# Optimization experiments

Measured on AMD Instinct MI355X. Metric: run time of the kernel, lower is better.

## Reference

```python
import jax, jax.numpy as jnp
import numpy as np

B, H, W, C = 16, 96, 96, 128
FOCAL_LEVEL = 3
FOCAL_WINDOW = 3
FOCAL_FACTOR = 2
LN_EPS = 1e-3  # keras LayerNormalization default epsilon


def dwconv_same(x, k):
    # x: [B,H,W,C], k: [kh,kw,1,C] depthwise kernel (feature_group_count=C)
    return jax.lax.conv_general_dilated(
        x, k, window_strides=(1, 1), padding='SAME',
        dimension_numbers=('NHWC', 'HWIO', 'NHWC'),
        feature_group_count=x.shape[-1])


def setup_inputs() -> dict:
    key = jax.random.key(0)
    ks = jax.random.split(key, 12)
    s = 0.02
    out_f = 2 * C + (FOCAL_LEVEL + 1)
    inp = {
        'x': jax.random.normal(ks[0], (B, H, W, C), dtype=jnp.float32),
        'Wf': jax.random.normal(ks[1], (C, out_f), dtype=jnp.float32) * s,
        'bf': jnp.zeros((out_f,), dtype=jnp.float32),
        'Wh': jax.random.normal(ks[2], (C, C), dtype=jnp.float32) * s,
        'bh': jnp.zeros((C,), dtype=jnp.float32),
        'gamma': jnp.ones((C,), dtype=jnp.float32),
        'beta': jnp.zeros((C,), dtype=jnp.float32),
        'Wp': jax.random.normal(ks[3], (C, C), dtype=jnp.float32) * s,
        'bp': jnp.zeros((C,), dtype=jnp.float32),
    }
    for l in range(FOCAL_LEVEL):
        kk = FOCAL_FACTOR * l + FOCAL_WINDOW  # 3, 5, 7
        inp[f'k{l}'] = jax.random.normal(ks[4 + l], (kk, kk, 1, C), dtype=jnp.float32) * s
    return inp


def reference(x, Wf, bf, k0, k1, k2, Wh, bh, gamma, beta, Wp, bp):
    gelu = lambda t: jax.nn.gelu(t, approximate=False)  # keras gelu is exact
    y = jnp.einsum('bhwc,cd->bhwd', x, Wf) + bf  # f(): [B,H,W,2C+L+1]
    q = y[..., :C]
    ctx = y[..., C:2 * C]
    gates = y[..., 2 * C:]  # [B,H,W,L+1]

    ctx_all = jnp.zeros_like(ctx)
    for l, k in enumerate((k0, k1, k2)):
        ctx = gelu(dwconv_same(ctx, k))
        ctx_all = ctx_all + ctx * gates[..., l:l + 1]

    ctx_global = gelu(jnp.mean(ctx, axis=(1, 2), keepdims=True))  # [B,1,1,C]
    ctx_all = ctx_all + ctx_global * gates[..., FOCAL_LEVEL:]

    modulator = jnp.einsum('bhwc,cd->bhwd', ctx_all, Wh) + bh  # 1x1 conv h()
    x_out = q * modulator

    # post-LN over channel dim
    mu = jnp.mean(x_out, axis=-1, keepdims=True)
    var = jnp.mean(jnp.square(x_out - mu), axis=-1, keepdims=True)
    x_out = (x_out - mu) * jax.lax.rsqrt(var + LN_EPS) * gamma + beta

    x_out = jnp.einsum('bhwc,cd->bhwd', x_out, Wp) + bp  # proj (dropout p=0)
    return x_out
```

## Files before the change

### kernel.cpp

```cpp
#include <hip/hip_runtime.h>
#include <math.h>

#define B_ 16
#define H_ 96
#define W_ 96
#define C_ 128
#define HW_ (H_*W_)
#define NTOK (B_*HW_)
#define NOUT 260

#define TH 16
#define TW 32
#define B0H 28
#define B0W 44
#define B1H 26
#define B1W 42
#define B2H 22
#define B2W 38

typedef unsigned short ushort_t;
typedef unsigned int uint_t;
typedef float f32x4 __attribute__((ext_vector_type(4)));
typedef float f32x2 __attribute__((ext_vector_type(2)));
typedef short bfrag __attribute__((ext_vector_type(8)));
typedef unsigned short us8 __attribute__((ext_vector_type(8)));

__device__ __forceinline__ float gelu_f(float t) {
    return 0.5f * t * (1.0f + erff(t * 0.7071067811865475f));
}
__device__ __forceinline__ float b2f(ushort_t u) {
    union { unsigned int i; float f; } t; t.i = (unsigned int)u << 16; return t.f;
}
__device__ __forceinline__ ushort_t f2b(float f) {
    union { float f; unsigned int i; } t; t.f = f;
    unsigned int lsb = (t.i >> 16) & 1u;
    t.i += 0x7fffu + lsb;
    return (ushort_t)(t.i >> 16);
}
__device__ __forceinline__ void unp2(uint_t u, float& a, float& b) {
    union { unsigned int i; float f; } x, y;
    x.i = u << 16; y.i = u & 0xffff0000u;
    a = x.f; b = y.f;
}
__device__ __forceinline__ void unp8(const uint4 v, float* f) {
    unp2(v.x, f[0], f[1]); unp2(v.y, f[2], f[3]);
    unp2(v.z, f[4], f[5]); unp2(v.w, f[6], f[7]);
}
__device__ __forceinline__ uint_t pk2(float a, float b) {
    return (uint_t)f2b(a) | ((uint_t)f2b(b) << 16);
}
__device__ __forceinline__ uint4 pk8(const float* f) {
    uint4 v;
    v.x = pk2(f[0], f[1]); v.y = pk2(f[2], f[3]);
    v.z = pk2(f[4], f[5]); v.w = pk2(f[6], f[7]);
    return v;
}
__device__ __forceinline__ f32x2 unp2p(uint_t u) {
    union { uint_t i; float f; } a, b;
    a.i = u << 16; b.i = u & 0xffff0000u;
    f32x2 r; r.x = a.f; r.y = b.f; return r;
}
__device__ __forceinline__ void unp8p(const uint4 v, f32x2* d) {
    d[0] = unp2p(v.x); d[1] = unp2p(v.y); d[2] = unp2p(v.z); d[3] = unp2p(v.w);
}

__device__ __forceinline__ void split8_to(const float* f,
                                          ushort_t* __restrict__ hdst,
                                          ushort_t* __restrict__ ldst) {
    us8 vh, vl;
    #pragma unroll
    for (int j = 0; j < 8; ++j) {
        const ushort_t h = f2b(f[j]);
        vh[j] = h;
        vl[j] = f2b(f[j] - b2f(h));
    }
    *(us8*)hdst = vh;
    *(us8*)ldst = vl;
}

__global__ __launch_bounds__(128) void pack_weights(
    const float* __restrict__ Wf, const float* __restrict__ Wh,
    const float* __restrict__ Wp, ushort_t* __restrict__ pk)
{
    const int n = blockIdx.x, mat = blockIdx.y, k = threadIdx.x;
    float v;
    if (mat == 0)      v = Wf[(size_t)k * NOUT + n];
    else if (mat == 1) v = Wf[(size_t)k * NOUT + C_ + n];
    else if (mat == 2) v = Wh[(size_t)k * C_ + n];
    else               v = Wp[(size_t)k * C_ + n];
    const ushort_t h = f2b(v);
    const ushort_t l = f2b(v - b2f(h));
    ushort_t* base = pk + (size_t)mat * (2 * C_ * C_);
    base[n * C_ + k] = h;
    base[C_ * C_ + n * C_ + k] = l;
}

template <bool A_LO>
__device__ __forceinline__ void mfma_gemm64(
    const ushort_t (*Ah)[136], const ushort_t (*Al)[136],
    const ushort_t* __restrict__ Bh, const ushort_t* __restrict__ Bl,
    int lane, int n0, f32x4 acc[4][2])
{
    const int ar = lane & 15;
    const int ak = (lane >> 4) << 3;
    #pragma unroll
    for (int kk = 0; kk < 4; ++kk) {
        const int kb = (kk << 5) + ak;
        const bfrag bh0 = *(const bfrag*)(Bh + (((n0      + ar) << 7) + kb));
        const bfrag bh1 = *(const bfrag*)(Bh + (((n0 + 16 + ar) << 7) + kb));
        const bfrag bl0 = *(const bfrag*)(Bl + (((n0      + ar) << 7) + kb));
        const bfrag bl1 = *(const bfrag*)(Bl + (((n0 + 16 + ar) << 7) + kb));
        #pragma unroll
        for (int m = 0; m < 4; ++m) {
            const bfrag ah = *(const bfrag*)&Ah[(m << 4) + ar][kb];
            if constexpr (A_LO) {
                const bfrag al = *(const bfrag*)&Al[(m << 4) + ar][kb];
                acc[m][0] = __builtin_amdgcn_mfma_f32_16x16x32_bf16(al, bh0, acc[m][0], 0, 0, 0);
                acc[m][1] = __builtin_amdgcn_mfma_f32_16x16x32_bf16(al, bh1, acc[m][1], 0, 0, 0);
            }
            acc[m][0] = __builtin_amdgcn_mfma_f32_16x16x32_bf16(ah, bl0, acc[m][0], 0, 0, 0);
            acc[m][1] = __builtin_amdgcn_mfma_f32_16x16x32_bf16(ah, bl1, acc[m][1], 0, 0, 0);
            acc[m][0] = __builtin_amdgcn_mfma_f32_16x16x32_bf16(ah, bh0, acc[m][0], 0, 0, 0);
            acc[m][1] = __builtin_amdgcn_mfma_f32_16x16x32_bf16(ah, bh1, acc[m][1], 0, 0, 0);
        }
    }
}

__device__ __forceinline__ void stage_split_f32(
    const float* __restrict__ src, int tid,
    ushort_t (*Ah)[136], ushort_t (*Al)[136])
{
    #pragma unroll
    for (int p = 0; p < 4; ++p) {
        const int i  = tid + (p << 8);
        const int t  = i >> 4;
        const int c8 = (i & 15) << 3;
        const float4 v0 = *(const float4*)(src + (size_t)t * C_ + c8);
        const float4 v1 = *(const float4*)(src + (size_t)t * C_ + c8 + 4);
        const float f[8] = {v0.x, v0.y, v0.z, v0.w, v1.x, v1.y, v1.z, v1.w};
        split8_to(f, &Ah[t][c8], &Al[t][c8]);
    }
}

__global__ __launch_bounds__(256) void gemm_ctx_gates_mfma(
    const float* __restrict__ x, const float* __restrict__ Wf,
    const float* __restrict__ bf, const ushort_t* __restrict__ pk,
    ushort_t* __restrict__ ctx, float* __restrict__ gates,
    float* __restrict__ csum)
{
    __shared__ ushort_t Abuf[2][64][136];
    const int tid  = threadIdx.x;
    const int tok0 = blockIdx.x * 64;
    const int lane = tid & 63;
    const int n0   = (tid >> 6) << 5;

    if (blockIdx.x < 8) csum[blockIdx.x * 256 + tid] = 0.0f;

    stage_split_f32(x + (size_t)tok0 * C_, tid, Abuf[0], Abuf[1]);
    __syncthreads();

    f32x4 acc[4][2] = {};
    {
        const ushort_t* Bh = pk + (size_t)1 * (2 * C_ * C_);
        const ushort_t* Bl = Bh + C_ * C_;
        mfma_gemm64<true>(Abuf[0], Abuf[1], Bh, Bl, lane, n0, acc);
    }

    {
        const int g = tid >> 6;
        float s = 0.f;
        #pragma unroll
        for (int k8 = 0; k8 < C_; k8 += 8) {
            const us8 vh = *(const us8*)&Abuf[0][lane][k8];
            const us8 vl = *(const us8*)&Abuf[1][lane][k8];
            #pragma unroll
            for (int j = 0; j < 8; ++j) {
                const float xv = b2f((ushort_t)vh[j]) + b2f((ushort_t)vl[j]);
                s += xv * Wf[(size_t)(k8 + j) * NOUT + 2*C_ + g];
            }
        }
        gates[(size_t)(tok0 + lane) * 4 + g] = s + bf[2*C_ + g];
    }
    __syncthreads();

    {
        const int ar = lane & 15;
        const int rg = (lane >> 4) << 2;
        #pragma unroll
        for (int n = 0; n < 2; ++n) {
            const int col = n0 + (n << 4) + ar;
            const float bias = bf[C_ + col];
            #pragma unroll
            for (int m = 0; m < 4; ++m)
                #pragma unroll
                for (int r = 0; r < 4; ++r)
                    Abuf[0][(m << 4) + rg + r][col] = f2b(acc[m][n][r] + bias);
        }
    }
    __syncthreads();

    #pragma unroll
    for (int p = 0; p < 4; ++p) {
        const int i  = tid + (p << 8);
        const int cg = i >> 6;
        const int t  = i & 63;
        *(uint4*)(ctx + (((size_t)cg * NTOK + tok0 + t) << 3))
            = *(const uint4*)&Abuf[0][t][cg << 3];
    }
}

__global__ __launch_bounds__(256, 4) void focal_conv_fused(
    const ushort_t* __restrict__ ctx_in,
    const float* __restrict__ k0w, const float* __restrict__ k1w,
    const float* __restrict__ k2w,
    const float* __restrict__ gates,
    ushort_t* __restrict__ ctx_all,
    float* __restrict__ csum)
{
    __shared__ uint4 bufA[B0H*B0W];
    __shared__ uint4 buf1[B1H*B1W];
    __shared__ float wts[(9+25+49)*8];

    const int tid  = threadIdx.x;
    const int cg   = blockIdx.x;
    const int tile = blockIdx.y;
    const int bb   = blockIdx.z;
    const int wt   = tile % 3, ht = tile / 3;
    const int c0   = cg << 3;
    const int h0   = ht * TH, w0 = wt * TW;

    if (tid < 166) {
        const int f = tid << 2;
        const float* src; int r;
        if (f < 72)       { r = f;       src = k0w; }
        else if (f < 272) { r = f - 72;  src = k1w; }
        else              { r = f - 272; src = k2w; }
        const int tap = r >> 3, off = r & 7;
        *(float4*)&wts[f] = *(const float4*)(src + tap * C_ + c0 + off);
    }

    const ushort_t* cin = ctx_in + (((size_t)cg * NTOK + (size_t)bb * HW_) << 3);
    for (int i = tid; i < B0H*B0W; i += 256) {
        const int r = i / B0W, q = i - r * B0W;
        const int hh = h0 - 6 + r, ww = w0 - 6 + q;
        uint4 v = make_uint4(0u, 0u, 0u, 0u);
        if ((unsigned)hh < (unsigned)H_ && (unsigned)ww < (unsigned)W_)
            v = *(const uint4*)(cin + ((size_t)(hh * W_ + ww) << 3));
        bufA[i] = v;
    }
    __syncthreads();

    {
        int iv[5], ecp[5], boff[5];
        #pragma unroll
        for (int p = 0; p < 5; ++p) {
            const int e = tid + (p << 8);
            iv[p] = (e < B1H*B1W);
            const int ec = iv[p] ? e : 0;
            ecp[p] = ec;
            boff[p] = (ec / B1W) * B0W + (ec % B1W);
        }
        f32x2 acc[5][4] = {};
        #pragma unroll 1
        for (int a = 0; a < 3; ++a) {
            #pragma unroll
            for (int b = 0; b < 3; ++b) {
                f32x2 wv[4];
                #pragma unroll
                for (int c = 0; c < 4; ++c)
                    wv[c] = *(const f32x2*)&wts[(a*3+b)*8 + 2*c];
                const int off = a * B0W + b;
                #pragma unroll
                for (int p = 0; p < 5; ++p) {
                    f32x2 d[4]; unp8p(bufA[boff[p] + off], d);
                    #pragma unroll
                    for (int c = 0; c < 4; ++c)
                        acc[p][c] = __builtin_elementwise_fma(d[c], wv[c], acc[p][c]);
                }
            }
        }
        __syncthreads();
        #pragma unroll
        for (int p = 0; p < 5; ++p) if (iv[p]) {
            float g[8];
            #pragma unroll
            for (int c = 0; c < 4; ++c) {
                g[2*c]   = gelu_f(acc[p][c].x);
                g[2*c+1] = gelu_f(acc[p][c].y);
            }
            buf1[ecp[p]] = pk8(g);
        }
    }
    __syncthreads();

    {
        int iv[4], ecp[4], boff[4];
        #pragma unroll
        for (int p = 0; p < 4; ++p) {
            const int e = tid + (p << 8);
            iv[p] = (e < B2H*B2W);
            const int ec = iv[p] ? e : 0;
            ecp[p] = ec;
            boff[p] = (ec / B2W) * B1W + (ec % B2W);
        }
        f32x2 acc[4][4] = {};
        #pragma unroll 1
        for (int a = 0; a < 5; ++a) {
            #pragma unroll
            for (int b = 0; b < 5; ++b) {
                f32x2 wv[4];
                #pragma unroll
                for (int c = 0; c < 4; ++c)
                    wv[c] = *(const f32x2*)&wts[72 + (a*5+b)*8 + 2*c];
                const int off = a * B1W + b;
                #pragma unroll
                for (int p = 0; p < 4; ++p) {
                    f32x2 d[4]; unp8p(buf1[boff[p] + off], d);
                    #pragma unroll
                    for (int c = 0; c < 4; ++c)
                        acc[p][c] = __builtin_elementwise_fma(d[c], wv[c], acc[p][c]);
                }
            }
        }
        __syncthreads();
        #pragma unroll
        for (int p = 0; p < 4; ++p) if (iv[p]) {
            float g[8];
            #pragma unroll
            for (int c = 0; c < 4; ++c) {
                g[2*c]   = gelu_f(acc[p][c].x);
                g[2*c+1] = gelu_f(acc[p][c].y);
            }
            bufA[ecp[p]] = pk8(g);
        }
    }
    __syncthreads();

    float lsum[8] = {};
    {
        const int th0 = tid >> 5, tw0 = tid & 31;
        f32x2 acc[2][4] = {};
        #pragma unroll 1
        for (int a = 0; a < 7; ++a) {
            #pragma unroll
            for (int b = 0; b < 7; ++b) {
                f32x2 wv[4];
                #pragma unroll
                for (int c = 0; c < 4; ++c)
                    wv[c] = *(const f32x2*)&wts[272 + (a*7+b)*8 + 2*c];
                #pragma unroll
                for (int p = 0; p < 2; ++p) {
                    const int th = th0 + (p << 3);
                    f32x2 d[4]; unp8p(bufA[(th + a)*B2W + (tw0 + b)], d);
                    #pragma unroll
                    for (int c = 0; c < 4; ++c)
                        acc[p][c] = __builtin_elementwise_fma(d[c], wv[c], acc[p][c]);
                }
            }
        }
        #pragma unroll
        for (int p = 0; p < 2; ++p) {
            const int th = th0 + (p << 3);
            float ctx3[8];
            #pragma unroll
            for (int c = 0; c < 4; ++c) {
                ctx3[2*c]   = gelu_f(acc[p][c].x);
                ctx3[2*c+1] = gelu_f(acc[p][c].y);
            }
            #pragma unroll
            for (int c = 0; c < 8; ++c) lsum[c] += ctx3[c];
            float d1[8]; unp8(buf1[(5+th)*B1W + (5+tw0)], d1);
            float d2[8]; unp8(bufA[(th+3)*B2W + (tw0+3)], d2);
            const size_t pix = (size_t)bb * HW_ + (size_t)(h0 + th) * W_ + (w0 + tw0);
            const float4 gt = *(const float4*)(gates + pix * 4);
            float o[8];
            #pragma unroll
            for (int c = 0; c < 8; ++c)
                o[c] = d1[c] * gt.x + d2[c] * gt.y + ctx3[c] * gt.z;
            *(uint4*)(ctx_all + pix * C_ + c0) = pk8(o);
        }
    }

    __syncthreads();
    float* red = (float*)bufA;
    #pragma unroll
    for (int c = 0; c < 8; ++c) red[c*256 + tid] = lsum[c];
    __syncthreads();
    for (int off = 128; off > 0; off >>= 1) {
        if (tid < off) {
            #pragma unroll
            for (int c = 0; c < 8; ++c)
                red[c*256 + tid] += red[c*256 + tid + off];
        }
        __syncthreads();
    }
    if (tid < 8) atomicAdd(&csum[bb * C_ + c0 + tid], red[tid * 256]);
}

__global__ __launch_bounds__(256) void mean_fin(
    const float* __restrict__ csum, float* __restrict__ cglob)
{
    const int i = blockIdx.x * 256 + threadIdx.x;
    if (i < B_ * C_) cglob[i] = gelu_f(csum[i] * (1.0f / (float)HW_));
}

__global__ __launch_bounds__(256) void modq_ln_mfma(
    const ushort_t* __restrict__ ctx_all, const float* __restrict__ cglob,
    const float* __restrict__ gates, const float* __restrict__ x,
    const ushort_t* __restrict__ pk, const float* __restrict__ bf,
    const float* __restrict__ bh, const float* __restrict__ gamma,
    const float* __restrict__ beta, ushort_t* __restrict__ xln)
{
    __shared__ ushort_t Abuf[2][64][136];
    __shared__ float mu_s[64];
    __shared__ float rs_s[64];
    float (*xs)[132] = (float(*)[132])&Abuf[0][0][0];

    const int tid  = threadIdx.x;
    const int tok0 = blockIdx.x * 64;
    const int bidx = tok0 / HW_;
    const int lane = tid & 63;
    const int n0   = (tid >> 6) << 5;

    #pragma unroll
    for (int p = 0; p < 4; ++p) {
        const int i  = tid + (p << 8);
        const int t  = i >> 4;
        const int c8 = (i & 15) << 3;
        const float g3 = gates[(size_t)(tok0 + t) * 4 + 3];
        const ushort4 u0 = *(const ushort4*)(ctx_all + (size_t)(tok0 + t) * C_ + c8);
        const ushort4 u1 = *(const ushort4*)(ctx_all + (size_t)(tok0 + t) * C_ + c8 + 4);
        const float4 g0 = *(const float4*)(cglob + bidx * C_ + c8);
        const float4 g1 = *(const float4*)(cglob + bidx * C_ + c8 + 4);
        const float f[8] = {
            b2f(u0.x) + g0.x * g3, b2f(u0.y) + g0.y * g3,
            b2f(u0.z) + g0.z * g3, b2f(u0.w) + g0.w * g3,
            b2f(u1.x) + g1.x * g3, b2f(u1.y) + g1.y * g3,
            b2f(u1.z) + g1.z * g3, b2f(u1.w) + g1.w * g3 };
        split8_to(f, &Abuf[0][t][c8], &Abuf[1][t][c8]);
    }
    __syncthreads();

    f32x4 am[4][2] = {};
    {
        const ushort_t* Bh2 = pk + (size_t)2 * (2 * C_ * C_);
        const ushort_t* Bl2 = Bh2 + C_ * C_;
        mfma_gemm64<true>(Abuf[0], Abuf[1], Bh2, Bl2, lane, n0, am);
    }
    __syncthreads();

    stage_split_f32(x + (size_t)tok0 * C_, tid, Abuf[0], Abuf[1]);
    __syncthreads();

    f32x4 aq[4][2] = {};
    {
        const ushort_t* Bh0 = pk;
        const ushort_t* Bl0 = Bh0 + C_ * C_;
        mfma_gemm64<true>(Abuf[0], Abuf[1], Bh0, Bl0, lane, n0, aq);
    }
    __syncthreads();

    {
        const int ar = lane & 15;
        const int rg = (lane >> 4) << 2;
        #pragma unroll
        for (int n = 0; n < 2; ++n) {
            const int col = n0 + (n << 4) + ar;
            const float bfv = bf[col];
            const float bhv = bh[col];
            #pragma unroll
            for (int m = 0; m < 4; ++m)
                #pragma unroll
                for (int r = 0; r < 4; ++r) {
                    const int row = (m << 4) + rg + r;
                    xs[row][col] = (aq[m][n][r] + bfv) * (am[m][n][r] + bhv);
                }
        }
    }
    __syncthreads();

    if (tid < 64) {
        float s = 0.f, s2 = 0.f;
        #pragma unroll
        for (int c = 0; c < C_; c += 4) {
            const float4 v = *(const float4*)&xs[tid][c];
            s  += v.x + v.y + v.z + v.w;
            s2 += v.x*v.x + v.y*v.y + v.z*v.z + v.w*v.w;
        }
        const float mu  = s * (1.0f / 128.0f);
        const float var = s2 * (1.0f / 128.0f) - mu * mu;
        mu_s[tid] = mu;
        rs_s[tid] = rsqrtf(var + 0.001f);
    }
    __syncthreads();

    {
        const int tt = tid >> 2;
        const int c0b = (tid & 3) << 5;
        const float mu = mu_s[tt], rs = rs_s[tt];
        ushort_t* op = xln + (size_t)(tok0 + tt) * C_;
        #pragma unroll
        for (int j = 0; j < 8; ++j) {
            const int c = c0b + (j << 2);
            const float4 v  = *(const float4*)&xs[tt][c];
            const float4 gm = *(const float4*)(gamma + c);
            const float4 bt = *(const float4*)(beta + c);
            ushort4 o;
            o.x = f2b((v.x - mu) * rs * gm.x + bt.x);
            o.y = f2b((v.y - mu) * rs * gm.y + bt.y);
            o.z = f2b((v.z - mu) * rs * gm.z + bt.z);
            o.w = f2b((v.w - mu) * rs * gm.w + bt.w);
            *(ushort4*)(op + c) = o;
        }
    }
}

__global__ __launch_bounds__(256) void gemm_out_mfma(
    const ushort_t* __restrict__ xln, const ushort_t* __restrict__ pk,
    const float* __restrict__ bp, float* __restrict__ out)
{
    __shared__ ushort_t Ah[64][136];
    const int tid  = threadIdx.x;
    const int tok0 = blockIdx.x * 64;
    const int lane = tid & 63;
    const int n0   = (tid >> 6) << 5;

    #pragma unroll
    for (int p = 0; p < 4; ++p) {
        const int i  = tid + (p << 8);
        const int t  = i >> 4;
        const int c8 = (i & 15) << 3;
        *(us8*)&Ah[t][c8] = *(const us8*)(xln + (size_t)(tok0 + t) * C_ + c8);
    }
    __syncthreads();

    f32x4 acc[4][2] = {};
    {
        const ushort_t* Bh3 = pk + (size_t)3 * (2 * C_ * C_);
        const ushort_t* Bl3 = Bh3 + C_ * C_;
        mfma_gemm64<false>(Ah, Ah, Bh3, Bl3, lane, n0, acc);
    }

    {
        const int ar = lane & 15;
        const int rg = (lane >> 4) << 2;
        #pragma unroll
        for (int n = 0; n < 2; ++n) {
            const int col = n0 + (n << 4) + ar;
            const float bpv = bp[col];
            #pragma unroll
            for (int m = 0; m < 4; ++m)
                #pragma unroll
                for (int r = 0; r < 4; ++r) {
                    const int row = (m << 4) + rg + r;
                    out[(size_t)(tok0 + row) * C_ + col] = acc[m][n][r] + bpv;
                }
        }
    }
}

extern "C" void kernel_launch(void* const* d_in, const int* in_sizes, int n_in,
                              void* d_out, int out_size, void* d_ws, size_t ws_size,
                              hipStream_t stream) {
    const float* x     = (const float*)d_in[0];
    const float* Wf    = (const float*)d_in[1];
    const float* bf    = (const float*)d_in[2];
    const float* Wh    = (const float*)d_in[3];
    const float* bh    = (const float*)d_in[4];
    const float* gamma = (const float*)d_in[5];
    const float* beta  = (const float*)d_in[6];
    const float* Wp    = (const float*)d_in[7];
    const float* bp    = (const float*)d_in[8];
    const float* k0    = (const float*)d_in[9];
    const float* k1    = (const float*)d_in[10];
    const float* k2    = (const float*)d_in[11];
    float* out = (float*)d_out;

    const size_t NC = (size_t)NTOK * C_;
    ushort_t* P0  = (ushort_t*)d_ws;
    ushort_t* ACC = P0 + NC;
    float* gates  = (float*)(ACC + NC);
    float* csum   = gates + (size_t)NTOK * 4;
    float* cglob  = csum + (size_t)B_ * C_;
    ushort_t* pkw = (ushort_t*)(cglob + (size_t)B_ * C_);

    pack_weights<<<dim3(C_, 4), 128, 0, stream>>>(Wf, Wh, Wp, pkw);
    gemm_ctx_gates_mfma<<<NTOK / 64, 256, 0, stream>>>(x, Wf, bf, pkw, P0, gates, csum);
    focal_conv_fused<<<dim3(C_/8, (H_/TH)*(W_/TW), B_), 256, 0, stream>>>(
        P0, k0, k1, k2, gates, ACC, csum);
    mean_fin<<<(B_ * C_ + 255) / 256, 256, 0, stream>>>(csum, cglob);
    modq_ln_mfma<<<NTOK / 64, 256, 0, stream>>>(ACC, cglob, gates, x, pkw, bf, bh, gamma, beta, P0);
    gemm_out_mfma<<<NTOK / 64, 256, 0, stream>>>(P0, pkw, bp, out);
}
```

Baseline: 426.6 us.

## Fuse LN and output GEMM, fold global context through Wh, MFMA gates

Merges the modulator/LN kernel with the output projection so the normalized activations stay in shared memory instead of going through a global round trip. The global context term is algebraically moved out of the ctx_all GEMM: gelu(mean) is multiplied by Wh once per batch and added as g3*whc, which lets the Wh GEMM use the bf16 ctx_all directly without the hi/lo split. The scalar gate dot products become a small MFMA against packed gate weights, and exact erf GELU is replaced by a polynomial approximation. This trades some accuracy, from the erf approximation and the dropped low-part split on the Wh input, for less memory traffic, fewer launches and less compute.

```diff
diff --git a/kernel.cpp b/kernel.cpp
--- a/kernel.cpp
+++ b/kernel.cpp
@@ -26,7 +26,18 @@
 typedef unsigned short us8 __attribute__((ext_vector_type(8)));
 
 __device__ __forceinline__ float gelu_f(float t) {
-    return 0.5f * t * (1.0f + erff(t * 0.7071067811865475f));
+    const float x  = t * 0.7071067811865475f;
+    const float ax = fabsf(x);
+    const float u  = __fdividef(1.0f, fmaf(0.3275911f, ax, 1.0f));
+    float p = fmaf(1.061405429f, u, -1.453152027f);
+    p = fmaf(p, u, 1.421413741f);
+    p = fmaf(p, u, -0.284496736f);
+    p = fmaf(p, u, 0.254829592f);
+    p = p * u;
+    const float e  = __expf(-ax * ax);
+    float er = fmaf(-p, e, 1.0f);
+    er = (x < 0.0f) ? -er : er;
+    return 0.5f * t * (1.0f + er);
 }
 __device__ __forceinline__ float b2f(ushort_t u) {
     union { unsigned int i; float f; } t; t.i = (unsigned int)u << 16; return t.f;
@@ -83,16 +94,19 @@
     const float* __restrict__ Wp, ushort_t* __restrict__ pk)
 {
     const int n = blockIdx.x, mat = blockIdx.y, k = threadIdx.x;
+    if (mat == 4 && n >= 16) return;
     float v;
     if (mat == 0)      v = Wf[(size_t)k * NOUT + n];
     else if (mat == 1) v = Wf[(size_t)k * NOUT + C_ + n];
     else if (mat == 2) v = Wh[(size_t)k * C_ + n];
-    else               v = Wp[(size_t)k * C_ + n];
+    else if (mat == 3) v = Wp[(size_t)k * C_ + n];
+    else               v = (n < 4) ? Wf[(size_t)k * NOUT + 2*C_ + n] : 0.0f;
     const ushort_t h = f2b(v);
     const ushort_t l = f2b(v - b2f(h));
     ushort_t* base = pk + (size_t)mat * (2 * C_ * C_);
+    const int lo_off = (mat == 4) ? 16 * C_ : C_ * C_;
     base[n * C_ + k] = h;
-    base[C_ * C_ + n * C_ + k] = l;
+    base[lo_off + n * C_ + k] = l;
 }
 
 template <bool A_LO>
@@ -143,8 +157,8 @@
 }
 
 __global__ __launch_bounds__(256) void gemm_ctx_gates_mfma(
-    const float* __restrict__ x, const float* __restrict__ Wf,
-    const float* __restrict__ bf, const ushort_t* __restrict__ pk,
+    const float* __restrict__ x, const float* __restrict__ bf,
+    const ushort_t* __restrict__ pk,
     ushort_t* __restrict__ ctx, float* __restrict__ gates,
     float* __restrict__ csum)
 {
@@ -167,19 +181,29 @@
     }
 
     {
-        const int g = tid >> 6;
-        float s = 0.f;
-        #pragma unroll
-        for (int k8 = 0; k8 < C_; k8 += 8) {
-            const us8 vh = *(const us8*)&Abuf[0][lane][k8];
-            const us8 vl = *(const us8*)&Abuf[1][lane][k8];
-            #pragma unroll
-            for (int j = 0; j < 8; ++j) {
-                const float xv = b2f((ushort_t)vh[j]) + b2f((ushort_t)vl[j]);
-                s += xv * Wf[(size_t)(k8 + j) * NOUT + 2*C_ + g];
-            }
-        }
-        gates[(size_t)(tok0 + lane) * 4 + g] = s + bf[2*C_ + g];
+        const int w  = tid >> 6;
+        const int ar = lane & 15;
+        const int ak = (lane >> 4) << 3;
+        const ushort_t* Gh = pk + (size_t)4 * (2 * C_ * C_);
+        const ushort_t* Gl = Gh + 16 * C_;
+        f32x4 gacc = {};
+        #pragma unroll
+        for (int kk = 0; kk < 4; ++kk) {
+            const int kb = (kk << 5) + ak;
+            const bfrag gh = *(const bfrag*)(Gh + ((ar << 7) + kb));
+            const bfrag gl = *(const bfrag*)(Gl + ((ar << 7) + kb));
+            const bfrag ah = *(const bfrag*)&Abuf[0][(w << 4) + ar][kb];
+            const bfrag al = *(const bfrag*)&Abuf[1][(w << 4) + ar][kb];
+            gacc = __builtin_amdgcn_mfma_f32_16x16x32_bf16(al, gh, gacc, 0, 0, 0);
+            gacc = __builtin_amdgcn_mfma_f32_16x16x32_bf16(ah, gl, gacc, 0, 0, 0);
+            gacc = __builtin_amdgcn_mfma_f32_16x16x32_bf16(ah, gh, gacc, 0, 0, 0);
+        }
+        if (ar < 4) {
+            const int rg = (lane >> 4) << 2;
+            #pragma unroll
+            for (int r = 0; r < 4; ++r)
+                gates[(size_t)(tok0 + (w << 4) + rg + r) * 4 + ar] = gacc[r] + bf[2*C_ + ar];
+        }
     }
     __syncthreads();
 
@@ -397,55 +421,61 @@
     if (tid < 8) atomicAdd(&csum[bb * C_ + c0 + tid], red[tid * 256]);
 }
 
-__global__ __launch_bounds__(256) void mean_fin(
-    const float* __restrict__ csum, float* __restrict__ cglob)
+__global__ __launch_bounds__(128) void glob_mod(
+    const float* __restrict__ csum, const float* __restrict__ Wh,
+    float* __restrict__ whc)
 {
-    const int i = blockIdx.x * 256 + threadIdx.x;
-    if (i < B_ * C_) cglob[i] = gelu_f(csum[i] * (1.0f / (float)HW_));
-}
-
-__global__ __launch_bounds__(256) void modq_ln_mfma(
-    const ushort_t* __restrict__ ctx_all, const float* __restrict__ cglob,
+    __shared__ float cg[128];
+    const int b = blockIdx.x, n = threadIdx.x;
+    cg[n] = gelu_f(csum[b * C_ + n] * (1.0f / (float)HW_));
+    __syncthreads();
+    float s = 0.f;
+    #pragma unroll 8
+    for (int k = 0; k < C_; ++k)
+        s = fmaf(cg[k], Wh[(size_t)k * C_ + n], s);
+    whc[b * C_ + n] = s;
+}
+
+__global__ __launch_bounds__(256) void modq_ln_out_mfma(
+    const ushort_t* __restrict__ ctx_all, const float* __restrict__ whc,
     const float* __restrict__ gates, const float* __restrict__ x,
     const ushort_t* __restrict__ pk, const float* __restrict__ bf,
     const float* __restrict__ bh, const float* __restrict__ gamma,
-    const float* __restrict__ beta, ushort_t* __restrict__ xln)
+    const float* __restrict__ beta, const float* __restrict__ bp,
+    float* __restrict__ out)
 {
     __shared__ ushort_t Abuf[2][64][136];
+    __shared__ float g3s[64];
+    __shared__ float whcs[128];
     __shared__ float mu_s[64];
     __shared__ float rs_s[64];
     float (*xs)[132] = (float(*)[132])&Abuf[0][0][0];
+    ushort_t (*xlnb)[136] = (ushort_t(*)[136])&Abuf[0][0][0];
 
     const int tid  = threadIdx.x;
     const int tok0 = blockIdx.x * 64;
     const int bidx = tok0 / HW_;
     const int lane = tid & 63;
     const int n0   = (tid >> 6) << 5;
+    const int ar   = lane & 15;
+    const int rg   = (lane >> 4) << 2;
 
     #pragma unroll
     for (int p = 0; p < 4; ++p) {
         const int i  = tid + (p << 8);
         const int t  = i >> 4;
         const int c8 = (i & 15) << 3;
-        const float g3 = gates[(size_t)(tok0 + t) * 4 + 3];
-        const ushort4 u0 = *(const ushort4*)(ctx_all + (size_t)(tok0 + t) * C_ + c8);
-        const ushort4 u1 = *(const ushort4*)(ctx_all + (size_t)(tok0 + t) * C_ + c8 + 4);
-        const float4 g0 = *(const float4*)(cglob + bidx * C_ + c8);
-        const float4 g1 = *(const float4*)(cglob + bidx * C_ + c8 + 4);
-        const float f[8] = {
-            b2f(u0.x) + g0.x * g3, b2f(u0.y) + g0.y * g3,
-            b2f(u0.z) + g0.z * g3, b2f(u0.w) + g0.w * g3,
-            b2f(u1.x) + g1.x * g3, b2f(u1.y) + g1.y * g3,
-            b2f(u1.z) + g1.z * g3, b2f(u1.w) + g1.w * g3 };
-        split8_to(f, &Abuf[0][t][c8], &Abuf[1][t][c8]);
-    }
+        *(us8*)&Abuf[0][t][c8] = *(const us8*)(ctx_all + (size_t)(tok0 + t) * C_ + c8);
+    }
+    if (tid < 64)           g3s[tid]        = gates[(size_t)(tok0 + tid) * 4 + 3];
+    else if (tid < 192)     whcs[tid - 64]  = whc[bidx * C_ + (tid - 64)];
     __syncthreads();
 
     f32x4 am[4][2] = {};
     {
         const ushort_t* Bh2 = pk + (size_t)2 * (2 * C_ * C_);
         const ushort_t* Bl2 = Bh2 + C_ * C_;
-        mfma_gemm64<true>(Abuf[0], Abuf[1], Bh2, Bl2, lane, n0, am);
+        mfma_gemm64<false>(Abuf[0], Abuf[0], Bh2, Bl2, lane, n0, am);
     }
     __syncthreads();
 
@@ -461,19 +491,19 @@
     __syncthreads();
 
     {
-        const int ar = lane & 15;
-        const int rg = (lane >> 4) << 2;
         #pragma unroll
         for (int n = 0; n < 2; ++n) {
             const int col = n0 + (n << 4) + ar;
             const float bfv = bf[col];
             const float bhv = bh[col];
+            const float whv = whcs[col];
             #pragma unroll
             for (int m = 0; m < 4; ++m)
                 #pragma unroll
                 for (int r = 0; r < 4; ++r) {
                     const int row = (m << 4) + rg + r;
-                    xs[row][col] = (aq[m][n][r] + bfv) * (am[m][n][r] + bhv);
+                    const float mod = am[m][n][r] + g3s[row] * whv + bhv;
+                    xs[row][col] = (aq[m][n][r] + bfv) * mod;
                 }
         }
     }
@@ -498,52 +528,33 @@
         const int tt = tid >> 2;
         const int c0b = (tid & 3) << 5;
         const float mu = mu_s[tt], rs = rs_s[tt];
-        ushort_t* op = xln + (size_t)(tok0 + tt) * C_;
+        uint_t xw[16];
         #pragma unroll
         for (int j = 0; j < 8; ++j) {
             const int c = c0b + (j << 2);
             const float4 v  = *(const float4*)&xs[tt][c];
             const float4 gm = *(const float4*)(gamma + c);
             const float4 bt = *(const float4*)(beta + c);
-            ushort4 o;
-            o.x = f2b((v.x - mu) * rs * gm.x + bt.x);
-            o.y = f2b((v.y - mu) * rs * gm.y + bt.y);
-            o.z = f2b((v.z - mu) * rs * gm.z + bt.z);
-            o.w = f2b((v.w - mu) * rs * gm.w + bt.w);
-            *(ushort4*)(op + c) = o;
-        }
-    }
-}
-
-__global__ __launch_bounds__(256) void gemm_out_mfma(
-    const ushort_t* __restrict__ xln, const ushort_t* __restrict__ pk,
-    const float* __restrict__ bp, float* __restrict__ out)
-{
-    __shared__ ushort_t Ah[64][136];
-    const int tid  = threadIdx.x;
-    const int tok0 = blockIdx.x * 64;
-    const int lane = tid & 63;
-    const int n0   = (tid >> 6) << 5;
-
-    #pragma unroll
-    for (int p = 0; p < 4; ++p) {
-        const int i  = tid + (p << 8);
-        const int t  = i >> 4;
-        const int c8 = (i & 15) << 3;
-        *(us8*)&Ah[t][c8] = *(const us8*)(xln + (size_t)(tok0 + t) * C_ + c8);
-    }
-    __syncthreads();
-
-    f32x4 acc[4][2] = {};
+            xw[2*j]   = pk2((v.x - mu) * rs * gm.x + bt.x,
+                            (v.y - mu) * rs * gm.y + bt.y);
+            xw[2*j+1] = pk2((v.z - mu) * rs * gm.z + bt.z,
+                            (v.w - mu) * rs * gm.w + bt.w);
+        }
+        __syncthreads();
+        #pragma unroll
+        for (int j = 0; j < 4; ++j)
+            *(uint4*)&xlnb[tt][c0b + (j << 3)] = *(uint4*)&xw[4*j];
+    }
+    __syncthreads();
+
+    f32x4 ao[4][2] = {};
     {
         const ushort_t* Bh3 = pk + (size_t)3 * (2 * C_ * C_);
         const ushort_t* Bl3 = Bh3 + C_ * C_;
-        mfma_gemm64<false>(Ah, Ah, Bh3, Bl3, lane, n0, acc);
-    }
-
-    {
-        const int ar = lane & 15;
-        const int rg = (lane >> 4) << 2;
+        mfma_gemm64<false>((const ushort_t(*)[136])xlnb,
+                           (const ushort_t(*)[136])xlnb, Bh3, Bl3, lane, n0, ao);
+    }
+    {
         #pragma unroll
         for (int n = 0; n < 2; ++n) {
             const int col = n0 + (n << 4) + ar;
@@ -553,7 +564,7 @@
                 #pragma unroll
                 for (int r = 0; r < 4; ++r) {
                     const int row = (m << 4) + rg + r;
-                    out[(size_t)(tok0 + row) * C_ + col] = acc[m][n][r] + bpv;
+                    out[(size_t)(tok0 + row) * C_ + col] = ao[m][n][r] + bpv;
                 }
         }
     }
@@ -581,14 +592,14 @@
     ushort_t* ACC = P0 + NC;
     float* gates  = (float*)(ACC + NC);
     float* csum   = gates + (size_t)NTOK * 4;
-    float* cglob  = csum + (size_t)B_ * C_;
-    ushort_t* pkw = (ushort_t*)(cglob + (size_t)B_ * C_);
-
-    pack_weights<<<dim3(C_, 4), 128, 0, stream>>>(Wf, Wh, Wp, pkw);
-    gemm_ctx_gates_mfma<<<NTOK / 64, 256, 0, stream>>>(x, Wf, bf, pkw, P0, gates, csum);
+    float* whc    = csum + (size_t)B_ * C_;
+    ushort_t* pkw = (ushort_t*)(whc + (size_t)B_ * C_);
+
+    pack_weights<<<dim3(C_, 5), 128, 0, stream>>>(Wf, Wh, Wp, pkw);
+    gemm_ctx_gates_mfma<<<NTOK / 64, 256, 0, stream>>>(x, bf, pkw, P0, gates, csum);
     focal_conv_fused<<<dim3(C_/8, (H_/TH)*(W_/TW), B_), 256, 0, stream>>>(
         P0, k0, k1, k2, gates, ACC, csum);
-    mean_fin<<<(B_ * C_ + 255) / 256, 256, 0, stream>>>(csum, cglob);
-    modq_ln_mfma<<<NTOK / 64, 256, 0, stream>>>(ACC, cglob, gates, x, pkw, bf, bh, gamma, beta, P0);
-    gemm_out_mfma<<<NTOK / 64, 256, 0, stream>>>(P0, pkw, bp, out);
-}
+    glob_mod<<<B_, 128, 0, stream>>>(csum, Wh, whc);
+    modq_ln_out_mfma<<<NTOK / 64, 256, 0, stream>>>(
+        ACC, whc, gates, x, pkw, bf, bh, gamma, beta, bp, out);
+}
```

Result: slower. 453.1 us (+6.2%).
